# Optimization experiments

Hardware: AMD Instinct MI355X
Metric: run time of the kernel (lower is better)

Reference implementation:

```python
import jax, jax.numpy as jnp
import numpy as np

H = 768      # hidden_size
NH = 12      # num_heads
HD = H // NH # head_dim = 64


def setup_inputs() -> dict:
    key = jax.random.key(0)
    k1, k2, k3 = jax.random.split(key, 3)
    x = jax.random.normal(k1, (4, 2048, H), dtype=jnp.float32)
    # nn.Linear weights are [out, in]; we store transposed [in, out] for x @ W
    w_qkv = jax.random.normal(k2, (H, 3 * H), dtype=jnp.float32) * (1.0 / np.sqrt(H))
    w_out = jax.random.normal(k3, (H, H), dtype=jnp.float32) * (1.0 / np.sqrt(H))
    return {"x": x, "w_qkv": w_qkv, "w_out": w_out}


def reference(x, w_qkv, w_out):
    B, S, _ = x.shape
    qkv = (x @ w_qkv).reshape(B, S, 3, NH, HD)
    qkv = jnp.transpose(qkv, (2, 0, 3, 1, 4))  # [3, B, NH, S, HD]
    q, k, v = qkv[0], qkv[1], qkv[2]
    scale = 1.0 / np.sqrt(HD)
    scores = jnp.einsum('bhqd,bhkd->bhqk', q, k) * scale  # [B,NH,S,S]
    causal = jnp.tril(jnp.ones((S, S), dtype=bool))
    scores = jnp.where(causal, scores, jnp.finfo(scores.dtype).min)
    attn = jax.nn.softmax(scores, axis=-1)
    out = jnp.einsum('bhqk,bhkd->bhqd', attn, v)          # [B,NH,S,HD]
    out = jnp.transpose(out, (0, 2, 1, 3)).reshape(B, S, H)
    return out @ w_out
```

## Files before the change

### kernel.cpp

```cpp
#include <hip/hip_runtime.h>
#include <type_traits>

#define S_LEN 2048
#define HID   768
#define NHEAD 12
#define HDIM  64
#define BATCH 4

typedef __attribute__((ext_vector_type(4))) float float4v;
typedef __attribute__((ext_vector_type(8))) short short8;
typedef __attribute__((ext_vector_type(4))) short short4v;
typedef __attribute__((ext_vector_type(2))) int int2v;

__device__ __forceinline__ short f2b(float f) {
  unsigned u = __float_as_uint(f);
  u += 0x7fff + ((u >> 16) & 1);
  return (short)(u >> 16);
}

__device__ __forceinline__ unsigned pkbf(float a, float b) {
#if __has_builtin(__builtin_amdgcn_cvt_pk_bf16_f32)
  typedef __attribute__((ext_vector_type(2))) __bf16 bf2;
  bf2 r = __builtin_amdgcn_cvt_pk_bf16_f32(a, b);
  return *(unsigned*)&r;
#else
  return ((unsigned)(unsigned short)f2b(a)) |
         (((unsigned)(unsigned short)f2b(b)) << 16);
#endif
}

__device__ __forceinline__ float fexp2(float x) {
#if __has_builtin(__builtin_amdgcn_exp2f)
  return __builtin_amdgcn_exp2f(x);
#else
  return __expf(x * 0.69314718056f);
#endif
}

__device__ __forceinline__ void g2l16(const short* g, short* l) {
  __builtin_amdgcn_global_load_lds(
      (const __attribute__((address_space(1))) void*)g,
      (__attribute__((address_space(3))) void*)l, 16, 0, 0);
}

__global__ __launch_bounds__(256) void prepass(const float* __restrict__ x,
                                               const float* __restrict__ w_qkv,
                                               const float* __restrict__ w_out,
                                               short* __restrict__ xb,
                                               short* __restrict__ wqkvT,
                                               short* __restrict__ woutT) {
  __shared__ float tile[64][65];
  const int blk = blockIdx.x;
  if (blk < 3072) {
    int i = blk * 2048 + threadIdx.x * 8;
    float4v a = *(const float4v*)&x[i];
    float4v b = *(const float4v*)&x[i + 4];
    short8 o;
#pragma unroll
    for (int j = 0; j < 4; j++) { o[j] = f2b(a[j]); o[j + 4] = f2b(b[j]); }
    *(short8*)&xb[i] = o;
    return;
  }
  const float* W; short* WT; int N_, scaleN, idx;
  if (blk < 3504) { idx = blk - 3072; W = w_qkv; WT = wqkvT; N_ = 3 * HID; scaleN = HID; }
  else            { idx = blk - 3504; W = w_out; WT = woutT; N_ = HID;     scaleN = 0;  }
  const int nblk = N_ / 64;
  const int n0 = (idx % nblk) * 64, k0 = (idx / nblk) * 64;
  const int tx = threadIdx.x & 63, ty = threadIdx.x >> 6;
#pragma unroll
  for (int r = 0; r < 16; r++) {
    int row = r * 4 + ty;
    tile[row][tx] = W[(size_t)(k0 + row) * N_ + n0 + tx];
  }
  __syncthreads();
#pragma unroll
  for (int r = 0; r < 16; r++) {
    int row = r * 4 + ty;
    float sc = (n0 + row < scaleN) ? 0.18033688011f : 1.0f;
    WT[(size_t)(n0 + row) * HID + k0 + tx] = f2b(tile[tx][row] * sc);
  }
}

template <int OUT>
__global__ __launch_bounds__(256) void gemm_bt(const short* __restrict__ A,
                                               const short* __restrict__ Bt,
                                               float* __restrict__ Cf,
                                               short* __restrict__ Cq,
                                               short* __restrict__ vT,
                                               int M, int N, int K) {
  __shared__ __align__(16) short As[128 * 32];
  __shared__ __align__(16) short Bs[128 * 32];
  const int tid = threadIdx.x;
  const int w = tid >> 6, lane = tid & 63;
  const int quad = lane >> 4, lm = lane & 15;
  const int m0 = blockIdx.y * 128, n0 = blockIdx.x * 128;
  const int mo = (w & 1) * 64, no = (w >> 1) * 64;

  float4v acc[4][4];
#pragma unroll
  for (int i = 0; i < 4; i++)
#pragma unroll
    for (int j = 0; j < 4; j++) acc[i][j] = (float4v)0.0f;

  const int srow = w * 32 + (lane >> 2);
  const int scol = (lane & 3) * 8;
  const short* Ag = A + (size_t)(m0 + srow) * K + scol;
  const short* Bg = Bt + (size_t)(n0 + srow) * K + scol;
  short* Al = &As[(w * 32) * 32];
  short* Bl = &Bs[(w * 32) * 32];

  for (int kb = 0; kb < K; kb += 32) {
    g2l16(Ag + kb, Al);
    g2l16(Ag + kb + (size_t)16 * K, Al + 16 * 32);
    g2l16(Bg + kb, Bl);
    g2l16(Bg + kb + (size_t)16 * K, Bl + 16 * 32);
    __syncthreads();

    short8 af[4], bf[4];
#pragma unroll
    for (int i = 0; i < 4; i++)
      af[i] = *(const short8*)&As[(mo + i * 16 + lm) * 32 + quad * 8];
#pragma unroll
    for (int j = 0; j < 4; j++)
      bf[j] = *(const short8*)&Bs[(no + j * 16 + lm) * 32 + quad * 8];
#pragma unroll
    for (int i = 0; i < 4; i++)
#pragma unroll
      for (int j = 0; j < 4; j++)
        acc[i][j] = __builtin_amdgcn_mfma_f32_16x16x32_bf16(af[i], bf[j], acc[i][j], 0, 0, 0);
    __syncthreads();
  }

  if constexpr (OUT == 0) {
#pragma unroll
    for (int i = 0; i < 4; i++)
#pragma unroll
      for (int j = 0; j < 4; j++)
#pragma unroll
        for (int r = 0; r < 4; r++)
          Cf[(size_t)(m0 + mo + i * 16 + quad * 4 + r) * N + n0 + no + j * 16 + lm] =
              acc[i][j][r];
  } else {
    if (n0 >= 2 * HID) {
      const int b = m0 >> 11;
      const int s0 = (m0 & 2047) + mo + quad * 4;
#pragma unroll
      for (int i = 0; i < 4; i++)
#pragma unroll
        for (int j = 0; j < 4; j++) {
          int col = n0 + no + j * 16 + lm - 2 * HID;
          int h = col >> 6, d = col & 63;
          short4v pv;
#pragma unroll
          for (int r = 0; r < 4; r++) pv[r] = f2b(acc[i][j][r]);
          *(short4v*)&vT[((size_t)(b * NHEAD + h) * HDIM + d) * S_LEN + s0 + i * 16] = pv;
        }
    } else {
#pragma unroll
      for (int i = 0; i < 4; i++)
#pragma unroll
        for (int j = 0; j < 4; j++)
#pragma unroll
          for (int r = 0; r < 4; r++)
            Cq[(size_t)(m0 + mo + i * 16 + quad * 4 + r) * (2 * HID) + n0 + no + j * 16 + lm] =
                f2b(acc[i][j][r]);
    }
  }
}

#define PST 72

__global__ __launch_bounds__(256) void attn_mfma(const short* __restrict__ qk,
                                                 const short* __restrict__ vT,
                                                 short* __restrict__ attnout) {
  __shared__ __align__(16) short Qs[128 * PST];
  __shared__ __align__(16) short Ks[64 * PST];
  __shared__ __align__(16) short Vt[64 * PST];
  __shared__ __align__(16) short Ps[4][16 * PST];

  const int tid = threadIdx.x;
  const int w = tid >> 6, lane = tid & 63;
  const int quad = lane >> 4, lm = lane & 15;
  const int bh = blockIdx.x, a = blockIdx.y;
  const int b = bh / NHEAD, h = bh % NHEAD;
  const int qtile[2] = {a, 31 - a};

  const size_t kbase = (size_t)(b * S_LEN) * (2 * HID) + HID + h * HDIM;
  const size_t vbase = (size_t)(b * NHEAD + h) * HDIM * S_LEN;

#pragma unroll
  for (int i = 0; i < 4; i++) {
    int flat = i * 256 + tid;
    int row = flat >> 3, c8 = (flat & 7) * 8;
    int grow = qtile[row >> 6] * 64 + (row & 63);
    *(short8*)&Qs[row * PST + c8] =
        *(const short8*)&qk[(size_t)(b * S_LEN + grow) * (2 * HID) + h * HDIM + c8];
  }

  float4v o_acc[2][4];
#pragma unroll
  for (int t = 0; t < 2; t++)
#pragma unroll
    for (int nt = 0; nt < 4; nt++) o_acc[t][nt] = (float4v)0.0f;
  float lsum[2][4];
#pragma unroll
  for (int t = 0; t < 2; t++)
#pragma unroll
    for (int r = 0; r < 4; r++) lsum[t][r] = 0.0f;

  const int ktmax = 32 - a;
  short8 kreg[2], vreg[2];

#define PREFETCH(KT)                                                               \
  {                                                                                \
    _Pragma("unroll") for (int i = 0; i < 2; i++) {                                \
      int flat = i * 256 + tid;                                                    \
      int p = flat >> 3, c8 = (flat & 7) * 8;                                      \
      int key = 4 * (p & 15) + (p >> 4);                                           \
      kreg[i] = *(const short8*)&qk[kbase + (size_t)((KT)*64 + key) * (2*HID) + c8]; \
      vreg[i] = *(const short8*)&vT[vbase + (size_t)p * S_LEN + (KT)*64 + c8];     \
    }                                                                              \
  }

  PREFETCH(0);

  for (int kt = 0; kt < ktmax; kt++) {
    __syncthreads();
#pragma unroll
    for (int i = 0; i < 2; i++) {
      int flat = i * 256 + tid;
      int p = flat >> 3, c8 = (flat & 7) * 8;
      *(short8*)&Ks[p * PST + c8] = kreg[i];
      *(short8*)&Vt[p * PST + c8] = vreg[i];
    }
    __syncthreads();
    if (kt + 1 < ktmax) PREFETCH(kt + 1);

#pragma unroll
    for (int t = 0; t < 2; t++) {
      if (t == 0 && kt > a) continue;
      float4v s_acc[4];
#pragma unroll
      for (int i = 0; i < 4; i++) s_acc[i] = (float4v)0.0f;
#pragma unroll
      for (int kb = 0; kb < 2; kb++) {
        short8 aq = *(const short8*)&Qs[(t * 64 + w * 16 + lm) * PST + kb * 32 + quad * 8];
#pragma unroll
        for (int nt = 0; nt < 4; nt++) {
          short8 bk = *(const short8*)&Ks[(nt * 16 + lm) * PST + kb * 32 + quad * 8];
          s_acc[nt] = __builtin_amdgcn_mfma_f32_16x16x32_bf16(aq, bk, s_acc[nt], 0, 0, 0);
        }
      }

      const bool diag = (kt == qtile[t]);
#pragma unroll
      for (int r = 0; r < 4; r++) {
        float e[4];
#pragma unroll
        for (int nt = 0; nt < 4; nt++) {
          float v = fexp2(s_acc[nt][r]);
          if (diag && (4 * lm + nt > w * 16 + quad * 4 + r)) v = 0.0f;
          lsum[t][r] += v;
          e[nt] = v;
        }
        int2v p2 = {(int)pkbf(e[0], e[1]), (int)pkbf(e[2], e[3])};
        *(int2v*)&Ps[w][(quad * 4 + r) * PST + lm * 4] = p2;
      }

#pragma unroll
      for (int kb = 0; kb < 2; kb++) {
        short8 ap = *(const short8*)&Ps[w][lm * PST + kb * 32 + quad * 8];
#pragma unroll
        for (int nt = 0; nt < 4; nt++) {
          short8 bv = *(const short8*)&Vt[(nt * 16 + lm) * PST + kb * 32 + quad * 8];
          o_acc[t][nt] = __builtin_amdgcn_mfma_f32_16x16x32_bf16(ap, bv, o_acc[t][nt], 0, 0, 0);
        }
      }
    }
  }

#pragma unroll
  for (int t = 0; t < 2; t++)
#pragma unroll
    for (int r = 0; r < 4; r++) {
#pragma unroll
      for (int off = 1; off < 16; off <<= 1)
        lsum[t][r] += __shfl_xor(lsum[t][r], off, 16);
      float inv = 1.0f / lsum[t][r];
      int rowg = b * S_LEN + qtile[t] * 64 + w * 16 + quad * 4 + r;
#pragma unroll
      for (int nt = 0; nt < 4; nt++)
        attnout[(size_t)rowg * HID + h * HDIM + nt * 16 + lm] =
            f2b(o_acc[t][nt][r] * inv);
    }
}

extern "C" void kernel_launch(void* const* d_in, const int* in_sizes, int n_in,
                              void* d_out, int out_size, void* d_ws, size_t ws_size,
                              hipStream_t stream) {
  const float* x     = (const float*)d_in[0];
  const float* w_qkv = (const float*)d_in[1];
  const float* w_out = (const float*)d_in[2];
  float* out = (float*)d_out;

  const int M = BATCH * S_LEN;
  short* qk     = (short*)d_ws;
  short* attn   = qk + (size_t)M * 2 * HID;
  short* vT     = attn + (size_t)M * HID;
  short* xb     = vT + (size_t)M * HID;
  short* wqkvT  = xb + (size_t)M * HID;
  short* woutT  = wqkvT + (size_t)(3 * HID) * HID;

  prepass<<<3648, 256, 0, stream>>>(x, w_qkv, w_out, xb, wqkvT, woutT);

  gemm_bt<1><<<dim3(3 * HID / 128, M / 128), 256, 0, stream>>>(
      xb, wqkvT, nullptr, qk, vT, M, 3 * HID, HID);
  attn_mfma<<<dim3(BATCH * NHEAD, S_LEN / 128), 256, 0, stream>>>(qk, vT, attn);
  gemm_bt<0><<<dim3(HID / 128, M / 128), 256, 0, stream>>>(
      attn, woutT, out, nullptr, nullptr, M, HID, HID);
}
```

Before: 209.2 us.

## Compute softmax row sums via MFMA with ones, hoist K/V fragments, set occupancy hint

Replaces the per-lane scalar accumulation of softmax denominators and the final cross-lane shuffle reduction with an extra MFMA against a vector of bf16 ones. As a side effect, the row sum now uses the bf16-rounded probabilities, which matches the values used in P·V. K and V fragments are loaded from shared memory once per key tile and reused across both query tiles, rather than reloaded for each. Prefetch addressing switches to incrementing pointers, and __launch_bounds__ gains a min-blocks hint of 3, which may constrain registers and cause spills given the larger fragment arrays held in registers.

```diff
diff --git a/kernel.cpp b/kernel.cpp
--- a/kernel.cpp
+++ b/kernel.cpp
@@ -170,9 +170,9 @@
 
 #define PST 72
 
-__global__ __launch_bounds__(256) void attn_mfma(const short* __restrict__ qk,
-                                                 const short* __restrict__ vT,
-                                                 short* __restrict__ attnout) {
+__global__ __launch_bounds__(256, 3) void attn_mfma(const short* __restrict__ qk,
+                                                    const short* __restrict__ vT,
+                                                    short* __restrict__ attnout) {
   __shared__ __align__(16) short Qs[128 * PST];
   __shared__ __align__(16) short Ks[64 * PST];
   __shared__ __align__(16) short Vt[64 * PST];
@@ -185,9 +185,6 @@
   const int b = bh / NHEAD, h = bh % NHEAD;
   const int qtile[2] = {a, 31 - a};
 
-  const size_t kbase = (size_t)(b * S_LEN) * (2 * HID) + HID + h * HDIM;
-  const size_t vbase = (size_t)(b * NHEAD + h) * HDIM * S_LEN;
-
 #pragma unroll
   for (int i = 0; i < 4; i++) {
     int flat = i * 256 + tid;
@@ -197,44 +194,59 @@
         *(const short8*)&qk[(size_t)(b * S_LEN + grow) * (2 * HID) + h * HDIM + c8];
   }
 
-  float4v o_acc[2][4];
-#pragma unroll
-  for (int t = 0; t < 2; t++)
+  float4v o_acc[2][4], o_sum[2];
+#pragma unroll
+  for (int t = 0; t < 2; t++) {
+    o_sum[t] = (float4v)0.0f;
 #pragma unroll
     for (int nt = 0; nt < 4; nt++) o_acc[t][nt] = (float4v)0.0f;
-  float lsum[2][4];
-#pragma unroll
-  for (int t = 0; t < 2; t++)
-#pragma unroll
-    for (int r = 0; r < 4; r++) lsum[t][r] = 0.0f;
+  }
+
+  short8 ones;
+#pragma unroll
+  for (int i = 0; i < 8; i++) ones[i] = (short)0x3F80;
 
   const int ktmax = 32 - a;
   short8 kreg[2], vreg[2];
 
-#define PREFETCH(KT)                                                               \
-  {                                                                                \
-    _Pragma("unroll") for (int i = 0; i < 2; i++) {                                \
-      int flat = i * 256 + tid;                                                    \
-      int p = flat >> 3, c8 = (flat & 7) * 8;                                      \
-      int key = 4 * (p & 15) + (p >> 4);                                           \
-      kreg[i] = *(const short8*)&qk[kbase + (size_t)((KT)*64 + key) * (2*HID) + c8]; \
-      vreg[i] = *(const short8*)&vT[vbase + (size_t)p * S_LEN + (KT)*64 + c8];     \
-    }                                                                              \
-  }
-
-  PREFETCH(0);
+  const int p0 = tid >> 3, c8g = (tid & 7) * 8;
+  const int key0 = 4 * (p0 & 15) + (p0 >> 4);
+  const short* kp = qk + (size_t)(b * S_LEN) * (2 * HID) + HID + h * HDIM +
+                    (size_t)key0 * (2 * HID) + c8g;
+  const short* vp = vT + (size_t)(b * NHEAD + h) * HDIM * S_LEN +
+                    (size_t)p0 * S_LEN + c8g;
+  const size_t KSTEP = (size_t)64 * 2 * HID;
+
+#define PREFETCH()                                        \
+  {                                                       \
+    kreg[0] = *(const short8*)kp;                         \
+    kreg[1] = *(const short8*)(kp + 2 * (2 * HID));       \
+    vreg[0] = *(const short8*)vp;                         \
+    vreg[1] = *(const short8*)(vp + 32 * S_LEN);          \
+    kp += KSTEP; vp += 64;                                \
+  }
+
+  PREFETCH();
 
   for (int kt = 0; kt < ktmax; kt++) {
     __syncthreads();
 #pragma unroll
     for (int i = 0; i < 2; i++) {
-      int flat = i * 256 + tid;
-      int p = flat >> 3, c8 = (flat & 7) * 8;
-      *(short8*)&Ks[p * PST + c8] = kreg[i];
-      *(short8*)&Vt[p * PST + c8] = vreg[i];
+      int p = p0 + i * 32;
+      *(short8*)&Ks[p * PST + c8g] = kreg[i];
+      *(short8*)&Vt[p * PST + c8g] = vreg[i];
     }
     __syncthreads();
-    if (kt + 1 < ktmax) PREFETCH(kt + 1);
+    if (kt + 1 < ktmax) PREFETCH();
+
+    short8 kf[2][4], vf[2][4];
+#pragma unroll
+    for (int kb = 0; kb < 2; kb++)
+#pragma unroll
+      for (int nt = 0; nt < 4; nt++) {
+        kf[kb][nt] = *(const short8*)&Ks[(nt * 16 + lm) * PST + kb * 32 + quad * 8];
+        vf[kb][nt] = *(const short8*)&Vt[(nt * 16 + lm) * PST + kb * 32 + quad * 8];
+      }
 
 #pragma unroll
     for (int t = 0; t < 2; t++) {
@@ -246,10 +258,8 @@
       for (int kb = 0; kb < 2; kb++) {
         short8 aq = *(const short8*)&Qs[(t * 64 + w * 16 + lm) * PST + kb * 32 + quad * 8];
 #pragma unroll
-        for (int nt = 0; nt < 4; nt++) {
-          short8 bk = *(const short8*)&Ks[(nt * 16 + lm) * PST + kb * 32 + quad * 8];
-          s_acc[nt] = __builtin_amdgcn_mfma_f32_16x16x32_bf16(aq, bk, s_acc[nt], 0, 0, 0);
-        }
+        for (int nt = 0; nt < 4; nt++)
+          s_acc[nt] = __builtin_amdgcn_mfma_f32_16x16x32_bf16(aq, kf[kb][nt], s_acc[nt], 0, 0, 0);
       }
 
       const bool diag = (kt == qtile[t]);
@@ -260,7 +270,6 @@
         for (int nt = 0; nt < 4; nt++) {
           float v = fexp2(s_acc[nt][r]);
           if (diag && (4 * lm + nt > w * 16 + quad * 4 + r)) v = 0.0f;
-          lsum[t][r] += v;
           e[nt] = v;
         }
         int2v p2 = {(int)pkbf(e[0], e[1]), (int)pkbf(e[2], e[3])};
@@ -271,10 +280,9 @@
       for (int kb = 0; kb < 2; kb++) {
         short8 ap = *(const short8*)&Ps[w][lm * PST + kb * 32 + quad * 8];
 #pragma unroll
-        for (int nt = 0; nt < 4; nt++) {
-          short8 bv = *(const short8*)&Vt[(nt * 16 + lm) * PST + kb * 32 + quad * 8];
-          o_acc[t][nt] = __builtin_amdgcn_mfma_f32_16x16x32_bf16(ap, bv, o_acc[t][nt], 0, 0, 0);
-        }
+        for (int nt = 0; nt < 4; nt++)
+          o_acc[t][nt] = __builtin_amdgcn_mfma_f32_16x16x32_bf16(ap, vf[kb][nt], o_acc[t][nt], 0, 0, 0);
+        o_sum[t] = __builtin_amdgcn_mfma_f32_16x16x32_bf16(ap, ones, o_sum[t], 0, 0, 0);
       }
     }
   }
@@ -283,10 +291,7 @@
   for (int t = 0; t < 2; t++)
 #pragma unroll
     for (int r = 0; r < 4; r++) {
-#pragma unroll
-      for (int off = 1; off < 16; off <<= 1)
-        lsum[t][r] += __shfl_xor(lsum[t][r], off, 16);
-      float inv = 1.0f / lsum[t][r];
+      float inv = 1.0f / o_sum[t][r];
       int rowg = b * S_LEN + qtile[t] * 64 + w * 16 + quad * 4 + r;
 #pragma unroll
       for (int nt = 0; nt < 4; nt++)
```

Result: slower. 250.1 us (+19.6%).
